# Optimization experiments

Hardware: AMD Instinct MI355X
Metric: run time of the kernel (lower is better)

Reference implementation:

```python
import jax, jax.numpy as jnp
import numpy as np


def setup_inputs() -> dict:
    key = jax.random.key(0)
    k1, k2 = jax.random.split(key)
    C, V, DEG = 256, 512, 6  # checks, variables, ~avg row degree (LDPC-sparse)
    H = (jax.random.uniform(k1, (C, V)) < DEG / V).astype(jnp.int32)
    llr = jax.random.normal(k2, (V,), dtype=jnp.float32) * 4.0  # LLR-scale values
    return {"llr": llr, "H": H, "max_iter": 2}


def reference(llr, H, max_iter):
    # Faithful translation of LDPCBeliefPropagation.forward, including its
    # sequential in-place update semantics (later node updates read earlier ones
    # within the same sweep).
    C, V = H.shape
    Hf = H.astype(jnp.float32)          # (C, V)
    Hb_T = (H == 1).T                   # (V, C) mask: Hb_T[v, j] = H[j, v]==1
    m_vtoc = jnp.ones((V, C), jnp.float32)
    m_ctov = jnp.zeros((C, V), jnp.float32)
    phi = lambda s: 2.0 * jnp.arctan(jnp.exp(0.5 * s))
    jidx = jnp.arange(V)

    for _ in range(max_iter):
        # --- variable->check pass: sequential over variable i ---
        # Original: m_vtoc[i, j] = sign(llr[i]) * prod_{v: H[j,v]==1} tanh(0.5*m_vtoc[v, j])
        # Step i writes row i; reads of column j see all rows < i already updated,
        # so we scan over i and recompute the masked column products each step.
        def p1(m, i):
            prod = jnp.prod(jnp.where(Hb_T, jnp.tanh(0.5 * m), 1.0), axis=0)  # (C,)
            return m.at[i].set(jnp.sign(llr[i]) * prod), None

        m_vtoc, _ = jax.lax.scan(p1, m_vtoc, jnp.arange(V))
        mv = m_vtoc

        # --- check->variable pass: sequential over check i ---
        # Original inner loop over j writes m_ctov[i, j] and reads column i of
        # m_ctov. Within fixed i, the only written element that is re-read is
        # (i, i) (written at j == i), so for j > i the sum gets the exact
        # correction H[i, j] * (v_new - old (i,i)). Bit-exact to the nested loop.
        def p2(m, i):
            col = m[:, i]                                  # (C,) old column i
            base = col @ Hf - mv[:, i]                     # (V,) masked sum - m_vtoc[j, i]
            v_new = phi(base[i])                           # value written at j == i
            adj = jnp.where(jidx > i, Hf[i] * (v_new - col[i]), 0.0)
            return m.at[i].set(phi(base + adj)), None

        m_ctov, _ = jax.lax.scan(p2, m_ctov, jnp.arange(C))

    soft = jnp.sign(llr) * jnp.prod(jnp.tanh(0.5 * m_ctov), axis=0)  # (V,)
    return jnp.where(soft > 0, 1, 0).astype(jnp.int32)[0:4]  # hardcoded [0:4] as in source
```

## Files before the change

kernel.cpp:

```cpp
#include <hip/hip_runtime.h>

#define CC 256
#define VV 512
#define MAXRD 26
#define MAXCD 18
#define PSTRIDE 27
#define RINGD 8
#define CLU 6

__device__ __forceinline__ float sgnf(float x) {
    return (x > 0.f) ? 1.f : ((x < 0.f) ? -1.f : 0.f);
}
__device__ __forceinline__ float phi_f(float x) {
    return 2.0f * atanf(expf(0.5f * x));
}
__device__ __forceinline__ void lds_barrier() {
    asm volatile("s_waitcnt lgkmcnt(0)" ::: "memory");
    __builtin_amdgcn_sched_barrier(0);
    __builtin_amdgcn_s_barrier();
    __builtin_amdgcn_sched_barrier(0);
}

__global__ __launch_bounds__(256)
void ldpc_bp5(const float* __restrict__ llr_g, const int* __restrict__ H_g,
              const int* __restrict__ it_g, int* __restrict__ out_g,
              float* __restrict__ ws)
{
    __shared__ float              llr_s[VV];
    __shared__ unsigned int       rsign[CC];
    __shared__ unsigned int       rzero[CC];
    __shared__ unsigned short     rdeg_s[CC];
    __shared__ float              Pst[CC][PSTRIDE];
    __shared__ unsigned short     clistT[MAXCD][CC];
    __shared__ unsigned short     cdeg_s[CC];
    __shared__ float              colbuf[2][257];
    __shared__ float              ring[RINGD][CC];
    __shared__ unsigned long long rowmask[CC][4];
    __shared__ unsigned char      rowpre[CC][4];

    const int j  = threadIdx.x;
    const int wv = j >> 6, ln = j & 63;
    float* __restrict__ mcT = ws;

    llr_s[j] = llr_g[j]; llr_s[j + CC] = llr_g[j + CC];
    __syncthreads();
    {
        int d = 0; unsigned int sb = 0, zb = 0;
        const int4* hrow = (const int4*)(H_g + j * VV);
        for (int g = 0; g < VV / 4; ++g) {
            int4 h = hrow[g]; const int v = g * 4;
            if (h.x) { if (d < MAXRD) { float l = llr_s[v+0]; sb |= (l < 0.f) << d; zb |= (l == 0.f) << d; } ++d; }
            if (h.y) { if (d < MAXRD) { float l = llr_s[v+1]; sb |= (l < 0.f) << d; zb |= (l == 0.f) << d; } ++d; }
            if (h.z) { if (d < MAXRD) { float l = llr_s[v+2]; sb |= (l < 0.f) << d; zb |= (l == 0.f) << d; } ++d; }
            if (h.w) { if (d < MAXRD) { float l = llr_s[v+3]; sb |= (l < 0.f) << d; zb |= (l == 0.f) << d; } ++d; }
        }
        rdeg_s[j] = (unsigned short)(d < MAXRD ? d : MAXRD);
        rsign[j] = sb; rzero[j] = zb;
    }
    {
        int d = 0;
        for (int c = 0; c < CC; ++c) {
            const int h = H_g[c * VV + j];
            const unsigned long long m = __ballot(h != 0);
            if (ln == 0) rowmask[c][wv] = m;
            if (h) { if (d < MAXCD) clistT[d][j] = (unsigned short)c; ++d; }
        }
        cdeg_s[j] = (unsigned short)(d < MAXCD ? d : MAXCD);
        for (int k = d; k < MAXCD; ++k) clistT[k][j] = 256;
    }
    colbuf[0][j] = 0.0f;
    if (j == 0) { colbuf[0][256] = 0.0f; colbuf[1][256] = 0.0f; }
    __syncthreads();
    {
        const int p1 = __popcll(rowmask[j][0]);
        const int p2 = p1 + __popcll(rowmask[j][1]);
        const int p3 = p2 + __popcll(rowmask[j][2]);
        rowpre[j][0] = 0; rowpre[j][1] = (unsigned char)p1;
        rowpre[j][2] = (unsigned char)p2; rowpre[j][3] = (unsigned char)p3;
    }
    const int cl0 = clistT[0][j], cl1 = clistT[1][j], cl2 = clistT[2][j];
    const int cl3 = clistT[3][j], cl4 = clistT[4][j], cl5 = clistT[5][j];
    const int cd  = cdeg_s[j];
    __syncthreads();

    const int   max_iter = it_g[0];
    const int   total    = max_iter * CC;
    const float T05      = tanhf(0.5f);
    const float sgj      = sgnf(llr_s[j]);

    float sv_base = 0.f, sv_bi = 0.f, sv_cbs = 0.f;
    int   sv_hv = 0;
    float val_prev = 0.f, fprod = 1.0f;

    auto STEP = [&](int T, float& pf_issue, float& pf_use) {
        const int s = T & 255;

        pf_issue = mcT[(size_t)((T + 4) & 255) * CC + j];

        if (T > 0) {
            float vnp;
            if (sv_hv) { float vnew = phi_f(sv_bi); vnp = phi_f(sv_base + (vnew - sv_cbs)); }
            else       vnp = phi_f(sv_base);
            val_prev = vnp;
            ring[(T - 1) & (RINGD - 1)][j] = vnp;
            mcT[(size_t)j * CC + ((T - 1) & 255)] = vnp;
            if (j < 4 && (T - 1) >= total - CC) fprod *= tanhf(0.5f * vnp);
        }

        if (s == 0) {
            const int pass = T >> 8;
            const int deg  = rdeg_s[j];
            const unsigned int sb = rsign[j], zb = rzero[j];
            float NP = 1.0f;
            for (int k = 0; k <= deg; ++k) {
                float P = NP;
                for (int idx = k; idx < deg; ++idx) {
                    float told;
                    if (pass == 0) told = T05;
                    else {
                        const float sg = ((zb >> idx) & 1u) ? 0.0f
                                       : (((sb >> idx) & 1u) ? -1.0f : 1.0f);
                        told = tanhf(0.5f * (sg * Pst[j][idx]));
                    }
                    P *= told;
                }
                Pst[j][k] = P;
                if (k < deg) {
                    const float sg = ((zb >> k) & 1u) ? 0.0f
                                   : (((sb >> k) & 1u) ? -1.0f : 1.0f);
                    NP *= tanhf(0.5f * (sg * P));
                }
            }
            lds_barrier();
        }

        const int Tc = T + 1;
        if (Tc < total) {
            const int X1 = Tc & 255;
            const int p  = T - ((T - j) & 255);
            if (p <= T - 2) {
                float v;
                if (p >= T - 8)    v = ring[p & (RINGD - 1)][X1];
                else if (p >= 0)   v = pf_use;
                else               v = 0.0f;
                colbuf[Tc & 1][j] = v;
            }
        }

        const int cur = T & 1;
        const unsigned long long rm = rowmask[s][wv];
        const int  kj  = (int)rowpre[s][wv] + __popcll(rm & ((1ull << ln) - 1ull));
        const bool hit = (rm >> ln) & 1ull;
        const float* cb = colbuf[cur];
        float sum = 0.0f;
        sum += cb[cl0]; sum += cb[cl1]; sum += cb[cl2];
        sum += cb[cl3]; sum += cb[cl4]; sum += cb[cl5];
        for (int k = CLU; k < cd; ++k) sum += cb[clistT[k][j]];
        const float base = sum - sgj * Pst[s][kj];
        const bool hv = hit && (j > s);
        float bi = 0.f, cbs = 0.f;
        if (hv) {
            float bsum = 0.0f;
            bsum += cb[clistT[0][s]]; bsum += cb[clistT[1][s]];
            bsum += cb[clistT[2][s]]; bsum += cb[clistT[3][s]];
            bsum += cb[clistT[4][s]]; bsum += cb[clistT[5][s]];
            const int cds = cdeg_s[s];
            for (int k = CLU; k < cds; ++k) bsum += cb[clistT[k][s]];
            const int ki = (int)rowpre[s][s >> 6]
                         + __popcll(rowmask[s][s >> 6] & ((1ull << (s & 63)) - 1ull));
            bi  = bsum - sgnf(llr_s[s]) * Pst[s][ki];
            cbs = cb[s];
        }
        sv_base = base; sv_bi = bi; sv_cbs = cbs; sv_hv = hv ? 1 : 0;

        if (Tc < total && j == (Tc & 255)) {
            float vo;
            if (hv) { float vnew = phi_f(bi); vo = phi_f(base + (vnew - cbs)); }
            else    vo = phi_f(base);
            colbuf[Tc & 1][s] = vo;
            colbuf[Tc & 1][(T - 1) & 255] = val_prev;
        }

        lds_barrier();
    };

    float p0 = 0.f, p1r = 0.f, p2r = 0.f, p3r = 0.f;
    #pragma unroll 1
    for (int T4 = 0; T4 < total; T4 += 4) {
        STEP(T4 + 0, p0,  p1r);
        STEP(T4 + 1, p1r, p2r);
        STEP(T4 + 2, p2r, p3r);
        STEP(T4 + 3, p3r, p0);
    }

    {
        float vnp;
        if (sv_hv) { float vnew = phi_f(sv_bi); vnp = phi_f(sv_base + (vnew - sv_cbs)); }
        else       vnp = phi_f(sv_base);
        if (j < 4) {
            fprod *= tanhf(0.5f * vnp);
            const float soft = sgj * fprod;
            out_g[j] = (soft > 0.0f) ? 1 : 0;
        }
    }
}

extern "C" void kernel_launch(void* const* d_in, const int* in_sizes, int n_in,
                              void* d_out, int out_size, void* d_ws, size_t ws_size,
                              hipStream_t stream) {
    const float* llr = (const float*)d_in[0];
    const int*   H   = (const int*)d_in[1];
    const int*   mi  = (const int*)d_in[2];
    int*         out = (int*)d_out;
    float*       ws  = (float*)d_ws;
    hipLaunchKernelGGL(ldpc_bp5, dim3(1), dim3(256), 0, stream,
                       llr, H, mi, out, ws);
}
```

Measured before the change: 582.9 us.

## Hoist LDS reads ahead of phi and defer one phi onto all threads

Moves the colbuf, ring and rowmask LDS loads to the top of each step so their latency overlaps the phi computation of the previous step's value. The designated thread now writes the raw pre-phi value into colbuf, and every thread applies phi itself and substitutes it when its check index matches. This shortens the serial chain through the single writing thread before the barrier. It also marks the workspace pointer as global address space so the compiler emits global memory instructions. The cost is redundant phi evaluation on all threads and an extra compare per gathered element.

```diff
diff --git a/kernel.cpp b/kernel.cpp
--- a/kernel.cpp
+++ b/kernel.cpp
@@ -8,6 +8,8 @@
 #define RINGD 8
 #define CLU 6
 
+typedef __attribute__((address_space(1))) float gfloat;
+
 __device__ __forceinline__ float sgnf(float x) {
     return (x > 0.f) ? 1.f : ((x < 0.f) ? -1.f : 0.f);
 }
@@ -22,7 +24,7 @@
 }
 
 __global__ __launch_bounds__(256)
-void ldpc_bp5(const float* __restrict__ llr_g, const int* __restrict__ H_g,
+void ldpc_bp7(const float* __restrict__ llr_g, const int* __restrict__ H_g,
               const int* __restrict__ it_g, int* __restrict__ out_g,
               float* __restrict__ ws)
 {
@@ -40,12 +42,11 @@
 
     const int j  = threadIdx.x;
     const int wv = j >> 6, ln = j & 63;
-    float* __restrict__ mcT = ws;
+    gfloat* __restrict__ mg = (gfloat*)ws;
 
     llr_s[j] = llr_g[j]; llr_s[j + CC] = llr_g[j + CC];
     __syncthreads();
-    {
-        int d = 0; unsigned int sb = 0, zb = 0;
+    {   int d = 0; unsigned int sb = 0, zb = 0;
         const int4* hrow = (const int4*)(H_g + j * VV);
         for (int g = 0; g < VV / 4; ++g) {
             int4 h = hrow[g]; const int v = g * 4;
@@ -57,8 +58,7 @@
         rdeg_s[j] = (unsigned short)(d < MAXRD ? d : MAXRD);
         rsign[j] = sb; rzero[j] = zb;
     }
-    {
-        int d = 0;
+    {   int d = 0;
         for (int c = 0; c < CC; ++c) {
             const int h = H_g[c * VV + j];
             const unsigned long long m = __ballot(h != 0);
@@ -71,8 +71,7 @@
     colbuf[0][j] = 0.0f;
     if (j == 0) { colbuf[0][256] = 0.0f; colbuf[1][256] = 0.0f; }
     __syncthreads();
-    {
-        const int p1 = __popcll(rowmask[j][0]);
+    {   const int p1 = __popcll(rowmask[j][0]);
         const int p2 = p1 + __popcll(rowmask[j][1]);
         const int p3 = p2 + __popcll(rowmask[j][2]);
         rowpre[j][0] = 0; rowpre[j][1] = (unsigned char)p1;
@@ -93,9 +92,19 @@
     float val_prev = 0.f, fprod = 1.0f;
 
     auto STEP = [&](int T, float& pf_issue, float& pf_use) {
-        const int s = T & 255;
-
-        pf_issue = mcT[(size_t)((T + 4) & 255) * CC + j];
+        const int s   = T & 255;
+        const int Tc  = T + 1;
+        const int X1  = Tc & 255;
+        const int sfx = (T >= 1) ? ((T - 1) & 255) : 511;
+
+        const float* cb = colbuf[T & 1];
+        const float g0 = cb[cl0], g1 = cb[cl1], g2 = cb[cl2];
+        const float g3 = cb[cl3], g4 = cb[cl4], g5 = cb[cl5];
+        const float craw = cb[sfx & 511];
+        const unsigned long long rm = rowmask[s][wv];
+        const int   p     = T - ((T - j) & 255);
+        const float ringv = ring[p & (RINGD - 1)][X1];
+        pf_issue = mg[((T + 4) & 255) * CC + j];
 
         if (T > 0) {
             float vnp;
@@ -103,7 +112,7 @@
             else       vnp = phi_f(sv_base);
             val_prev = vnp;
             ring[(T - 1) & (RINGD - 1)][j] = vnp;
-            mcT[(size_t)j * CC + ((T - 1) & 255)] = vnp;
+            mg[j * CC + ((T - 1) & 255)] = vnp;
             if (j < 4 && (T - 1) >= total - CC) fprod *= tanhf(0.5f * vnp);
         }
 
@@ -134,38 +143,33 @@
             lds_barrier();
         }
 
-        const int Tc = T + 1;
-        if (Tc < total) {
-            const int X1 = Tc & 255;
-            const int p  = T - ((T - j) & 255);
-            if (p <= T - 2) {
-                float v;
-                if (p >= T - 8)    v = ring[p & (RINGD - 1)][X1];
-                else if (p >= 0)   v = pf_use;
-                else               v = 0.0f;
-                colbuf[Tc & 1][j] = v;
-            }
-        }
-
-        const int cur = T & 1;
-        const unsigned long long rm = rowmask[s][wv];
         const int  kj  = (int)rowpre[s][wv] + __popcll(rm & ((1ull << ln) - 1ull));
         const bool hit = (rm >> ln) & 1ull;
-        const float* cb = colbuf[cur];
+        const float ph = phi_f(craw);
+        const float t0 = (cl0 == sfx) ? ph : g0;
+        const float t1 = (cl1 == sfx) ? ph : g1;
+        const float t2 = (cl2 == sfx) ? ph : g2;
+        const float t3 = (cl3 == sfx) ? ph : g3;
+        const float t4 = (cl4 == sfx) ? ph : g4;
+        const float t5 = (cl5 == sfx) ? ph : g5;
         float sum = 0.0f;
-        sum += cb[cl0]; sum += cb[cl1]; sum += cb[cl2];
-        sum += cb[cl3]; sum += cb[cl4]; sum += cb[cl5];
-        for (int k = CLU; k < cd; ++k) sum += cb[clistT[k][j]];
+        sum += t0; sum += t1; sum += t2; sum += t3; sum += t4; sum += t5;
+        for (int k = CLU; k < cd; ++k) {
+            const int ci = clistT[k][j];
+            float t = cb[ci]; if (ci == sfx) t = ph;
+            sum += t;
+        }
         const float base = sum - sgj * Pst[s][kj];
         const bool hv = hit && (j > s);
         float bi = 0.f, cbs = 0.f;
         if (hv) {
             float bsum = 0.0f;
-            bsum += cb[clistT[0][s]]; bsum += cb[clistT[1][s]];
-            bsum += cb[clistT[2][s]]; bsum += cb[clistT[3][s]];
-            bsum += cb[clistT[4][s]]; bsum += cb[clistT[5][s]];
             const int cds = cdeg_s[s];
-            for (int k = CLU; k < cds; ++k) bsum += cb[clistT[k][s]];
+            for (int k = 0; k < cds; ++k) {
+                const int ci = clistT[k][s];
+                float t = cb[ci]; if (ci == sfx) t = ph;
+                bsum += t;
+            }
             const int ki = (int)rowpre[s][s >> 6]
                          + __popcll(rowmask[s][s >> 6] & ((1ull << (s & 63)) - 1ull));
             bi  = bsum - sgnf(llr_s[s]) * Pst[s][ki];
@@ -173,12 +177,21 @@
         }
         sv_base = base; sv_bi = bi; sv_cbs = cbs; sv_hv = hv ? 1 : 0;
 
-        if (Tc < total && j == (Tc & 255)) {
-            float vo;
-            if (hv) { float vnew = phi_f(bi); vo = phi_f(base + (vnew - cbs)); }
-            else    vo = phi_f(base);
-            colbuf[Tc & 1][s] = vo;
-            colbuf[Tc & 1][(T - 1) & 255] = val_prev;
+        if (Tc < total) {
+            if (p <= T - 2) {
+                float v;
+                if (p >= T - 8)    v = ringv;
+                else if (p >= 0)   v = pf_use;
+                else               v = 0.0f;
+                colbuf[Tc & 1][j] = v;
+            }
+            if (j == X1) {
+                float rawv;
+                if (hv) { float vnew = phi_f(bi); rawv = base + (vnew - cbs); }
+                else    rawv = base;
+                colbuf[Tc & 1][s] = rawv;
+                colbuf[Tc & 1][(T - 1) & 255] = val_prev;
+            }
         }
 
         lds_barrier();
@@ -213,6 +226,6 @@
     const int*   mi  = (const int*)d_in[2];
     int*         out = (int*)d_out;
     float*       ws  = (float*)d_ws;
-    hipLaunchKernelGGL(ldpc_bp5, dim3(1), dim3(256), 0, stream,
+    hipLaunchKernelGGL(ldpc_bp7, dim3(1), dim3(256), 0, stream,
                        llr, H, mi, out, ws);
 }
```

Result: slower. 648.1 us (+11.2%).
